# Kernel tuning notes

Hardware: AMD Instinct MI355X
Metric: run time of the kernel (lower is better)

Reference implementation:

```python
import jax, jax.numpy as jnp
import numpy as np

B, T, V, E = 1024, 100, 9173, 100
H1, H2 = 128, 512


def _gru(x, k, rk, b):
    # Keras GRU v2 (reset_after=True). x: [B,T,D], k: [D,3H], rk: [H,3H], b: [2,3H]
    bi, br = b[0], b[1]
    xs = jnp.swapaxes(jnp.einsum('btd,dh->bth', x, k) + bi, 0, 1)  # [T,B,3H]
    H = rk.shape[0]
    h0 = jnp.zeros((x.shape[0], H), x.dtype)

    def step(h, xt):
        inner = h @ rk + br
        xz, xr, xh = jnp.split(xt, 3, -1)
        rz, rr, rh = jnp.split(inner, 3, -1)
        z = jax.nn.sigmoid(xz + rz)
        r = jax.nn.sigmoid(xr + rr)
        hh = jnp.tanh(xh + r * rh)
        h = z * h + (1.0 - z) * hh
        return h, h

    _, ys = jax.lax.scan(step, h0, xs)
    return jnp.swapaxes(ys, 0, 1)  # [B,T,H]


def _lstm(x, k, rk, b, reverse=False):
    # Keras LSTM, gate order i,f,c,o. x: [B,T,D], k: [D,4H], rk: [H,4H], b: [4H]
    if reverse:
        x = x[:, ::-1]
    xs = jnp.swapaxes(jnp.einsum('btd,dh->bth', x, k) + b, 0, 1)  # [T,B,4H]
    H = rk.shape[0]
    Bb = x.shape[0]
    carry0 = (jnp.zeros((Bb, H), x.dtype), jnp.zeros((Bb, H), x.dtype))

    def step(carry, xt):
        h, c = carry
        g = xt + h @ rk
        i, f, cc, o = jnp.split(g, 4, -1)
        c = jax.nn.sigmoid(f) * c + jax.nn.sigmoid(i) * jnp.tanh(cc)
        h = jax.nn.sigmoid(o) * jnp.tanh(c)
        return (h, c), h

    _, ys = jax.lax.scan(step, carry0, xs)
    ys = jnp.swapaxes(ys, 0, 1)
    if reverse:
        ys = ys[:, ::-1]  # Bidirectional re-reverses backward outputs
    return ys


def setup_inputs() -> dict:
    key = jax.random.key(0)
    ks = jax.random.split(key, 32)
    s = 0.05
    p = {}
    p['text'] = jax.random.randint(ks[0], (B, T), 0, V)
    p['upvote'] = jax.random.normal(ks[1], (B, 1), jnp.float32)
    p['emb'] = s * jax.random.normal(ks[2], (V, E), jnp.float32)
    # forward GRU(128)
    p['gf_k'] = s * jax.random.normal(ks[3], (E, 3 * H1), jnp.float32)
    p['gf_rk'] = s * jax.random.normal(ks[4], (H1, 3 * H1), jnp.float32)
    p['gf_b'] = s * jax.random.normal(ks[5], (2, 3 * H1), jnp.float32)
    # backward LSTM(128)
    p['lb_k'] = s * jax.random.normal(ks[6], (E, 4 * H1), jnp.float32)
    p['lb_rk'] = s * jax.random.normal(ks[7], (H1, 4 * H1), jnp.float32)
    p['lb_b'] = s * jax.random.normal(ks[8], (4 * H1,), jnp.float32)
    # GRU(512) on concat(256)
    p['g2_k'] = s * jax.random.normal(ks[9], (2 * H1, 3 * H2), jnp.float32)
    p['g2_rk'] = s * jax.random.normal(ks[10], (H2, 3 * H2), jnp.float32)
    p['g2_b'] = s * jax.random.normal(ks[11], (2, 3 * H2), jnp.float32)
    # LSTM(512)
    p['l2_k'] = s * jax.random.normal(ks[12], (H2, 4 * H2), jnp.float32)
    p['l2_rk'] = s * jax.random.normal(ks[13], (H2, 4 * H2), jnp.float32)
    p['l2_b'] = s * jax.random.normal(ks[14], (4 * H2,), jnp.float32)
    # dense heads
    p['fc1_w'] = s * jax.random.normal(ks[15], (1, 512), jnp.float32)
    p['fc1_b'] = jnp.zeros((512,), jnp.float32)
    p['d1_w'] = s * jax.random.normal(ks[16], (1024, 64), jnp.float32)
    p['d1_b'] = jnp.zeros((64,), jnp.float32)
    p['d2_w'] = s * jax.random.normal(ks[17], (64, 512), jnp.float32)
    p['d2_b'] = jnp.zeros((512,), jnp.float32)
    p['d3_w'] = s * jax.random.normal(ks[18], (512, 128), jnp.float32)
    p['d3_b'] = jnp.zeros((128,), jnp.float32)
    p['rat_w'] = s * jax.random.normal(ks[19], (128, 5), jnp.float32)
    p['rat_b'] = jnp.zeros((5,), jnp.float32)
    p['rec_w'] = s * jax.random.normal(ks[20], (128, 1), jnp.float32)
    p['rec_b'] = jnp.zeros((1,), jnp.float32)
    return p


def reference(text, upvote, emb, gf_k, gf_rk, gf_b, lb_k, lb_rk, lb_b,
              g2_k, g2_rk, g2_b, l2_k, l2_rk, l2_b,
              fc1_w, fc1_b, d1_w, d1_b, d2_w, d2_b, d3_w, d3_b,
              rat_w, rat_b, rec_w, rec_b):
    x = emb[text]                                   # [B,T,E]
    fwd = _gru(x, gf_k, gf_rk, gf_b)                # [B,T,128]
    bwd = _lstm(x, lb_k, lb_rk, lb_b, reverse=True)  # [B,T,128]
    x1 = jnp.concatenate([fwd, bwd], -1)            # [B,T,256]
    x1 = _gru(x1, g2_k, g2_rk, g2_b)                # [B,T,512]
    x1 = _lstm(x1, l2_k, l2_rk, l2_b)               # [B,T,512]
    x1 = jnp.mean(x1, axis=1)                       # GlobalAveragePooling1D
    x2 = jax.nn.relu(upvote @ fc1_w + fc1_b)        # [B,512]
    h = jnp.concatenate([x1, x2], -1)               # [B,1024]
    h = jax.nn.relu(h @ d1_w + d1_b)
    h = jax.nn.relu(h @ d2_w + d2_b)
    h = jax.nn.relu(h @ d3_w + d3_b)
    rating = jax.nn.softmax(h @ rat_w + rat_b, axis=-1)
    recommend = jax.nn.sigmoid(h @ rec_w + rec_b)
    return rating, recommend
```

## Files before the change

kernel.cpp:

```cpp
#include <hip/hip_runtime.h>

typedef __attribute__((ext_vector_type(8))) short bf16x8;
typedef __attribute__((ext_vector_type(4))) float f32x4;

#define MFMA(a, b, c) __builtin_amdgcn_mfma_f32_16x16x32_bf16((a), (b), (c), 0, 0, 0)

__device__ inline short f2bf(float f) {
  unsigned u = __builtin_bit_cast(unsigned, f);
  u += 0x7fffu + ((u >> 16) & 1u);
  return (short)(u >> 16);
}
__device__ inline float bf2f(short s) {
  unsigned u = ((unsigned)(unsigned short)s) << 16;
  return __builtin_bit_cast(float, u);
}
__device__ inline float sigm(float x) { return 1.f / (1.f + expf(-x)); }

#define VM_DRAIN() asm volatile("s_waitcnt vmcnt(0)" ::: "memory")

__device__ __forceinline__ void sc_load16(const char* g0, const char* g1,
                                          const char* l0, const char* l1,
                                          bf16x8* rg, bf16x8* rl) {
  asm volatile(
      "global_load_dwordx4 %0, %16, off sc0 sc1\n\t"
      "global_load_dwordx4 %1, %16, off offset:1024 sc0 sc1\n\t"
      "global_load_dwordx4 %2, %16, off offset:2048 sc0 sc1\n\t"
      "global_load_dwordx4 %3, %16, off offset:3072 sc0 sc1\n\t"
      "global_load_dwordx4 %4, %17, off sc0 sc1\n\t"
      "global_load_dwordx4 %5, %17, off offset:1024 sc0 sc1\n\t"
      "global_load_dwordx4 %6, %17, off offset:2048 sc0 sc1\n\t"
      "global_load_dwordx4 %7, %17, off offset:3072 sc0 sc1\n\t"
      "global_load_dwordx4 %8, %18, off sc0 sc1\n\t"
      "global_load_dwordx4 %9, %18, off offset:1024 sc0 sc1\n\t"
      "global_load_dwordx4 %10, %18, off offset:2048 sc0 sc1\n\t"
      "global_load_dwordx4 %11, %18, off offset:3072 sc0 sc1\n\t"
      "global_load_dwordx4 %12, %19, off sc0 sc1\n\t"
      "global_load_dwordx4 %13, %19, off offset:1024 sc0 sc1\n\t"
      "global_load_dwordx4 %14, %19, off offset:2048 sc0 sc1\n\t"
      "global_load_dwordx4 %15, %19, off offset:3072 sc0 sc1\n\t"
      "s_waitcnt vmcnt(0)"
      : "=&v"(rg[0]), "=&v"(rg[1]), "=&v"(rg[2]), "=&v"(rg[3]),
        "=&v"(rg[4]), "=&v"(rg[5]), "=&v"(rg[6]), "=&v"(rg[7]),
        "=&v"(rl[0]), "=&v"(rl[1]), "=&v"(rl[2]), "=&v"(rl[3]),
        "=&v"(rl[4]), "=&v"(rl[5]), "=&v"(rl[6]), "=&v"(rl[7])
      : "v"(g0), "v"(g1), "v"(l0), "v"(l1)
      : "memory");
}

__device__ __forceinline__ void store_short_sys(short* p, short v) {
  int vi = (int)(unsigned short)v;
  asm volatile("global_store_short %0, %1, off sc0 sc1" :: "v"(p), "v"(vi) : "memory");
}

#define B_SZ 1024
#define T_SZ 100

#define O_GFK   0u
#define O_GFRK  (O_GFK  + 98304u)
#define O_LBK   (O_GFRK + 98304u)
#define O_LBRK  (O_LBK  + 131072u)
#define O_G2    (O_LBRK + 131072u)
#define O_L2    (O_G2   + 2359296u)
#define O_X     (O_L2   + 4194304u)
#define O_X1    (O_X    + 26214400u)
#define O_HG    (O_X1   + 52428800u)
#define O_HL    (O_HG   + 2097152u)
#define O_BAR   (O_HL   + 2097152u)
#define O_MS    (O_BAR  + 2097152u)
#define O_HGH   (O_MS   + 2097152u)
#define O_HLH   (O_HGH  + 105906176u)
#define WS_NEED (O_HLH + 105906176u)

__global__ void pack_b(const float* __restrict__ s1, int K1,
                       const float* __restrict__ s2, int K1p,
                       int Kp, int N, short* __restrict__ dst) {
  int i = blockIdx.x * 256 + threadIdx.x;
  int total = N * Kp;
  if (i >= total) return;
  int v = i & 7, c = (i >> 3) & 15, r = i >> 7;
  int kb8 = Kp >> 3;
  int kb = r % kb8, nt = r / kb8;
  int k = kb * 8 + v, col = nt * 16 + c;
  float val;
  if (k < K1p) val = (k < K1) ? s1[k * N + col] : 0.f;
  else         val = s2[(k - K1p) * N + col];
  dst[i] = f2bf(val);
}

__global__ void embed_k(const int* __restrict__ text, const float* __restrict__ emb,
                        short* __restrict__ x) {
  int i = blockIdx.x * 256 + threadIdx.x;
  if (i >= B_SZ * T_SZ * 128) return;
  int col = i & 127, bt = i >> 7;
  float v = 0.f;
  if (col < 100) v = emb[text[bt] * 100 + col];
  x[i] = f2bf(v);
}

__global__ __launch_bounds__(512) void layer1_k(
    const short* __restrict__ x, const short* __restrict__ gfk,
    const short* __restrict__ gfrk, const float* __restrict__ gfb,
    const short* __restrict__ lbk, const short* __restrict__ lbrk,
    const float* __restrict__ lbb, short* __restrict__ x1) {
  __shared__ __attribute__((aligned(16))) short rkl[65536];
  __shared__ __attribute__((aligned(16))) short xst[16 * 136];
  __shared__ __attribute__((aligned(16))) short hst[16 * 136];
  const int wgid = blockIdx.x;
  const bool gru = wgid < 64;
  const int b0 = (gru ? wgid : wgid - 64) * 16;
  const int tid = threadIdx.x, lane = tid & 63, w = tid >> 6;
  const int c = lane & 15, g = lane >> 4;
  const int NS = gru ? 3 : 4;

  for (int i = tid; i < 16 * 136; i += 512) hst[i] = 0;

  const bf16x8* kp = (const bf16x8*)(gru ? gfk : lbk);
  const bf16x8* rpg = (const bf16x8*)(gru ? gfrk : lbrk);
  {
    bf16x8* rl8 = (bf16x8*)rkl;
    int n8 = gru ? 6144 : 8192;
    for (int i = tid; i < n8; i += 512) rl8[i] = rpg[i];
  }
  const bf16x8* rp = (const bf16x8*)rkl;

  bf16x8 kf[4][4];
  #pragma unroll
  for (int s = 0; s < 4; ++s)
    if (s < NS)
      #pragma unroll
      for (int ks = 0; ks < 4; ++ks)
        kf[s][ks] = kp[((s * 8 + w) * 16 + 4 * ks + g) * 16 + c];

  const int col = w * 16 + c;
  float bz = 0, br_ = 0, bxh = 0, brh = 0, bi_ = 0, bf_ = 0, bc_ = 0, bo_ = 0;
  if (gru) {
    bz  = gfb[col]       + gfb[384 + col];
    br_ = gfb[128 + col] + gfb[512 + col];
    bxh = gfb[256 + col];
    brh = gfb[640 + col];
  } else {
    bi_ = lbb[col]; bf_ = lbb[128 + col]; bc_ = lbb[256 + col]; bo_ = lbb[384 + col];
  }

  float hreg[4] = {0.f, 0.f, 0.f, 0.f};
  float cst[4]  = {0.f, 0.f, 0.f, 0.f};

  for (int tt = 0; tt < T_SZ; ++tt) {
    const int t = gru ? tt : (T_SZ - 1 - tt);
    __syncthreads();
    if (tid < 256) {
      int row = tid >> 4, ch = tid & 15;
      *(bf16x8*)&xst[row * 136 + ch * 8] =
          *(const bf16x8*)&x[((b0 + row) * T_SZ + t) * 128 + ch * 8];
    }
    __syncthreads();

    f32x4 acc[4];
    #pragma unroll
    for (int s = 0; s < 4; ++s) acc[s] = (f32x4){0.f, 0.f, 0.f, 0.f};

    bf16x8 ax[4], ah[4];
    #pragma unroll
    for (int ks = 0; ks < 4; ++ks) {
      ax[ks] = *(const bf16x8*)&xst[c * 136 + ks * 32 + g * 8];
      ah[ks] = *(const bf16x8*)&hst[c * 136 + ks * 32 + g * 8];
    }
    #pragma unroll
    for (int s = 0; s < 4; ++s) {
      if (s < NS) {
        int dst = (gru && s == 2) ? 3 : s;
        #pragma unroll
        for (int ks = 0; ks < 4; ++ks) {
          acc[s] = MFMA(ax[ks], kf[s][ks], acc[s]);
          bf16x8 bh = rp[((s * 8 + w) * 16 + 4 * ks + g) * 16 + c];
          acc[dst] = MFMA(ah[ks], bh, acc[dst]);
        }
      }
    }
    __syncthreads();

    if (gru) {
      #pragma unroll
      for (int j = 0; j < 4; ++j) {
        float z  = sigm(acc[0][j] + bz);
        float r  = sigm(acc[1][j] + br_);
        float hh = tanhf(acc[2][j] + bxh + r * (acc[3][j] + brh));
        float hn = z * hreg[j] + (1.f - z) * hh;
        hreg[j] = hn;
        short hb = f2bf(hn);
        int row = 4 * g + j;
        hst[row * 136 + col] = hb;
        x1[((b0 + row) * T_SZ + t) * 256 + col] = hb;
      }
    } else {
      #pragma unroll
      for (int j = 0; j < 4; ++j) {
        float i_ = acc[0][j] + bi_;
        float f_ = acc[1][j] + bf_;
        float cc = acc[2][j] + bc_;
        float o_ = acc[3][j] + bo_;
        float cn = sigm(f_) * cst[j] + sigm(i_) * tanhf(cc);
        cst[j] = cn;
        float hn = sigm(o_) * tanhf(cn);
        short hb = f2bf(hn);
        int row = 4 * g + j;
        hst[row * 136 + col] = hb;
        x1[((b0 + row) * T_SZ + t) * 256 + 128 + col] = hb;
      }
    }
  }
}

__device__ __forceinline__ void gbar16(unsigned* bar, int grp, int gen) {
  VM_DRAIN();
  __syncthreads();
  if (threadIdx.x == 0) {
    unsigned want = (unsigned)(gen + 1);
    unsigned* cnt = bar + grp * 32;
    unsigned* rel = cnt + 16;
    unsigned o = __hip_atomic_fetch_add(cnt, 1u, __ATOMIC_RELAXED, __HIP_MEMORY_SCOPE_AGENT);
    if (o == want * 16u - 1u) {
      __hip_atomic_store(rel, want, __ATOMIC_RELAXED, __HIP_MEMORY_SCOPE_AGENT);
    } else {
      unsigned tries = 0;
      while (__hip_atomic_load(rel, __ATOMIC_RELAXED, __HIP_MEMORY_SCOPE_AGENT) < want) {
        __builtin_amdgcn_s_sleep(2);
        if (++tries > (1u << 22)) break;
      }
    }
  }
  __syncthreads();
}

__global__ __launch_bounds__(512, 2) void persist2_k(
    const short* __restrict__ x1, const short* __restrict__ G2p, const float* __restrict__ g2b,
    const short* __restrict__ L2p, const float* __restrict__ l2b,
    short* __restrict__ hg, short* __restrict__ hl,
    short* __restrict__ hgH, short* __restrict__ hlH,
    float* __restrict__ msum, unsigned* __restrict__ bar, int mode) {
  __shared__ __attribute__((aligned(16))) short Asm[65536];
  float* XA  = (float*)Asm;
  float* XB  = (float*)&Asm[32768];

  const int wgid = blockIdx.x;
  const int rowwg = wgid & 15, colwg = wgid >> 4;
  const int b0 = rowwg * 64;
  const int tid = threadIdx.x, w = tid >> 6, lane = tid & 63;
  const int c = lane & 15, g = lane >> 4;
  const int c7 = c & 7;
  const int ehc = lane & 31;
  const int er0 = w * 8 + (lane >> 5) * 4;
  const int hcg = colwg * 32 + ehc;

  const float bz  = g2b[hcg] + g2b[1536 + hcg];
  const float br_ = g2b[512 + hcg] + g2b[2048 + hcg];
  const float bxh = g2b[1024 + hcg];
  const float brh = g2b[2560 + hcg];
  const float bi_ = l2b[hcg], bf_ = l2b[512 + hcg];
  const float bc_ = l2b[1024 + hcg], bo_ = l2b[1536 + hcg];

  const bf16x8* Gv  = (const bf16x8*)G2p;
  const bf16x8* L2v = (const bf16x8*)L2p;
  const int gw = w >> 1, ghf = w & 1;
  const int gntg = gw * 32 + colwg * 2 + ghf;
  const int lgate = w & 3, lkh = w >> 2;

  float creg[4] = {0.f, 0.f, 0.f, 0.f};
  float mreg[4] = {0.f, 0.f, 0.f, 0.f};

  for (int k = 0; k <= 100; ++k) {
    const short* hg_rd = mode ? hgH + (size_t)k * 524288
                              : hg + (size_t)((k + 1) & 1) * 524288;
    const short* hl_rd = mode ? hlH + (size_t)(k >= 1 ? k - 1 : 0) * 524288
                              : hl + (size_t)(k & 1) * 524288;

    if (k < 100) {
      const bf16x8* x1v = (const bf16x8*)x1;
      #pragma unroll
      for (int it = 0; it < 4; ++it) {
        int idx = it * 512 + tid;
        int row = idx >> 5, cx = idx & 31;
        *(bf16x8*)&Asm[32768 + row * 256 + ((cx ^ (row & 7)) << 3)] =
            x1v[((size_t)(b0 + row) * T_SZ + k) * 32 + cx];
      }
    }

    bf16x8 rg[8], rl[8];
    {
      const char* bg = (const char*)hg_rd + (size_t)(b0 + w * 8) * 1024 + (size_t)lane * 16;
      const char* bl = (const char*)hl_rd + (size_t)(b0 + w * 8) * 1024 + (size_t)lane * 16;
      if (mode) {
        #pragma unroll
        for (int q = 0; q < 8; ++q) rg[q] = *(const bf16x8*)(bg + q * 1024);
        #pragma unroll
        for (int q = 0; q < 8; ++q) rl[q] = *(const bf16x8*)(bl + q * 1024);
      } else {
        sc_load16(bg, bg + 4096, bl, bl + 4096, rg, rl);
      }
    }
    #pragma unroll
    for (int q = 0; q < 8; ++q)
      *(bf16x8*)&Asm[(w * 8 + q) * 512 + ((lane ^ q) << 3)] = rg[q];
    __syncthreads();

    if (k < 100) {
      f32x4 acc[4], acch[4];
      if (w < 6) {
        #pragma unroll
        for (int m = 0; m < 4; ++m) {
          acc[m] = (f32x4){0.f, 0.f, 0.f, 0.f};
          acch[m] = (f32x4){0.f, 0.f, 0.f, 0.f};
        }
        #pragma unroll 6
        for (int ks = 0; ks < 24; ++ks) {
          bf16x8 b = Gv[((size_t)gntg * 96 + 4 * ks + g) * 16 + c];
          bf16x8 a[4];
          #pragma unroll
          for (int m = 0; m < 4; ++m) {
            int row = m * 16 + c;
            a[m] = (ks < 8)
                ? *(const bf16x8*)&Asm[32768 + row * 256 + (((ks * 4 + g) ^ c7) << 3)]
                : *(const bf16x8*)&Asm[row * 512 + ((((ks - 8) * 4 + g) ^ c7) << 3)];
          }
          if (w >= 4 && ks >= 8) {
            #pragma unroll
            for (int m = 0; m < 4; ++m) acch[m] = MFMA(a[m], b, acch[m]);
          } else {
            #pragma unroll
            for (int m = 0; m < 4; ++m) acc[m] = MFMA(a[m], b, acc[m]);
          }
        }
      }
      __syncthreads();

      if (w < 6) {
        #pragma unroll
        for (int m = 0; m < 4; ++m)
          #pragma unroll
          for (int j = 0; j < 4; ++j) {
            int row = m * 16 + 4 * g + j;
            if (gw < 2) XB[(gw * 64 + row) * 36 + ghf * 16 + c] = acc[m][j];
            else {
              XB[(128 + row) * 36 + ghf * 16 + c] = acc[m][j];
              XB[(192 + row) * 36 + ghf * 16 + c] = acch[m][j];
            }
          }
      }
      __syncthreads();

      short* hgw = mode ? hgH + (size_t)(k + 1) * 524288
                        : hg + (size_t)(k & 1) * 524288;
      #pragma unroll
      for (int j = 0; j < 4; ++j) {
        int r = er0 + j;
        int xi = r * 36 + ehc;
        float z  = sigm(XB[xi] + bz);
        float rr = sigm(XB[xi + 2304] + br_);
        float hh = tanhf(XB[xi + 4608] + bxh + rr * (XB[xi + 6912] + brh));
        float hold = bf2f(Asm[r * 512 + (((hcg >> 3) ^ (r & 7)) << 3) + (hcg & 7)]);
        float hn = z * hold + (1.f - z) * hh;
        store_short_sys(&hgw[(size_t)(b0 + r) * 512 + hcg], f2bf(hn));
      }
      __syncthreads();
    }

    if (k >= 1) {
      #pragma unroll
      for (int q = 0; q < 8; ++q)
        *(bf16x8*)&Asm[32768 + (w * 8 + q) * 512 + ((lane ^ q) << 3)] = rl[q];
      __syncthreads();

      f32x4 acc[4][2];
      #pragma unroll
      for (int m = 0; m < 4; ++m)
        #pragma unroll
        for (int n = 0; n < 2; ++n) acc[m][n] = (f32x4){0.f, 0.f, 0.f, 0.f};

      const int abase = lkh ? 32768 : 0;
      #pragma unroll
      for (int ks = 0; ks < 16; ++ks) {
        bf16x8 a[4];
        #pragma unroll
        for (int m = 0; m < 4; ++m) {
          int row = m * 16 + c;
          a[m] = *(const bf16x8*)&Asm[abase + row * 512 + (((ks * 4 + g) ^ c7) << 3)];
        }
        #pragma unroll
        for (int m = 0; m < 4; ++m)
          #pragma unroll
          for (int n = 0; n < 2; ++n) {
            bf16x8 b = L2v[((size_t)(lgate * 32 + colwg * 2 + n) * 128 +
                            4 * (lkh * 16 + ks) + g) * 16 + c];
            acc[m][n] = MFMA(a[m], b, acc[m][n]);
          }
      }
      __syncthreads();

      float* Xp = lkh ? XB : XA;
      #pragma unroll
      for (int m = 0; m < 4; ++m)
        #pragma unroll
        for (int n = 0; n < 2; ++n)
          #pragma unroll
          for (int j = 0; j < 4; ++j)
            Xp[(lgate * 64 + m * 16 + 4 * g + j) * 36 + n * 16 + c] = acc[m][n][j];
      __syncthreads();

      short* hlw = mode ? hlH + (size_t)k * 524288
                        : hl + (size_t)((k + 1) & 1) * 524288;
      #pragma unroll
      for (int j = 0; j < 4; ++j) {
        int r = er0 + j;
        int xi = r * 36 + ehc;
        float i_ = XA[xi]        + XB[xi]        + bi_;
        float f_ = XA[xi + 2304] + XB[xi + 2304] + bf_;
        float cc = XA[xi + 4608] + XB[xi + 4608] + bc_;
        float o_ = XA[xi + 6912] + XB[xi + 6912] + bo_;
        float cn = sigm(f_) * creg[j] + sigm(i_) * tanhf(cc);
        creg[j] = cn;
        float hn = sigm(o_) * tanhf(cn);
        mreg[j] += hn;
        store_short_sys(&hlw[(size_t)(b0 + r) * 512 + hcg], f2bf(hn));
      }
    }

    gbar16(bar, rowwg, k);
  }

  #pragma unroll
  for (int j = 0; j < 4; ++j)
    msum[(size_t)(b0 + er0 + j) * 512 + hcg] = mreg[j];
}

__global__ __launch_bounds__(256) void head_k(
    const float* __restrict__ msum, const float* __restrict__ upv,
    const float* __restrict__ fc1w, const float* __restrict__ fc1b,
    const float* __restrict__ d1w, const float* __restrict__ d1b,
    const float* __restrict__ d2w, const float* __restrict__ d2b,
    const float* __restrict__ d3w, const float* __restrict__ d3b,
    const float* __restrict__ rw, const float* __restrict__ rb,
    const float* __restrict__ cw, const float* __restrict__ cb,
    float* __restrict__ out) {
  __shared__ float h[1024], o1[64], o2[512], o3[128], lg[8];
  const int b = blockIdx.x, tid = threadIdx.x;
  const float u = upv[b];
  for (int i = tid; i < 512; i += 256) {
    h[i] = msum[b * 512 + i] * 0.01f;
    float v = u * fc1w[i] + fc1b[i];
    h[512 + i] = v > 0.f ? v : 0.f;
  }
  __syncthreads();
  if (tid < 64) {
    float a = d1b[tid];
    for (int i = 0; i < 1024; ++i) a += h[i] * d1w[i * 64 + tid];
    o1[tid] = a > 0.f ? a : 0.f;
  }
  __syncthreads();
  for (int j = tid; j < 512; j += 256) {
    float a = d2b[j];
    for (int i = 0; i < 64; ++i) a += o1[i] * d2w[i * 512 + j];
    o2[j] = a > 0.f ? a : 0.f;
  }
  __syncthreads();
  if (tid < 128) {
    float a = d3b[tid];
    for (int i = 0; i < 512; ++i) a += o2[i] * d3w[i * 128 + tid];
    o3[tid] = a > 0.f ? a : 0.f;
  }
  __syncthreads();
  if (tid < 5) {
    float a = rb[tid];
    for (int i = 0; i < 128; ++i) a += o3[i] * rw[i * 5 + tid];
    lg[tid] = a;
  }
  if (tid == 5) {
    float a = cb[0];
    for (int i = 0; i < 128; ++i) a += o3[i] * cw[i];
    out[5120 + b] = 1.f / (1.f + expf(-a));
  }
  __syncthreads();
  if (tid == 0) {
    float m = lg[0];
    for (int j = 1; j < 5; ++j) m = fmaxf(m, lg[j]);
    float e[5], s = 0.f;
    for (int j = 0; j < 5; ++j) { e[j] = expf(lg[j] - m); s += e[j]; }
    for (int j = 0; j < 5; ++j) out[b * 5 + j] = e[j] / s;
  }
}

extern "C" void kernel_launch(void* const* d_in, const int* in_sizes, int n_in,
                              void* d_out, int out_size, void* d_ws, size_t ws_size,
                              hipStream_t stream) {
  const int*   text  = (const int*)  d_in[0];
  const float* upv   = (const float*)d_in[1];
  const float* emb   = (const float*)d_in[2];
  const float* gf_k  = (const float*)d_in[3];
  const float* gf_rk = (const float*)d_in[4];
  const float* gf_b  = (const float*)d_in[5];
  const float* lb_k  = (const float*)d_in[6];
  const float* lb_rk = (const float*)d_in[7];
  const float* lb_b  = (const float*)d_in[8];
  const float* g2_k  = (const float*)d_in[9];
  const float* g2_rk = (const float*)d_in[10];
  const float* g2_b  = (const float*)d_in[11];
  const float* l2_k  = (const float*)d_in[12];
  const float* l2_rk = (const float*)d_in[13];
  const float* l2_b  = (const float*)d_in[14];
  const float* fc1_w = (const float*)d_in[15];
  const float* fc1_b = (const float*)d_in[16];
  const float* d1_w  = (const float*)d_in[17];
  const float* d1_b  = (const float*)d_in[18];
  const float* d2_w  = (const float*)d_in[19];
  const float* d2_b  = (const float*)d_in[20];
  const float* d3_w  = (const float*)d_in[21];
  const float* d3_b  = (const float*)d_in[22];
  const float* rat_w = (const float*)d_in[23];
  const float* rat_b = (const float*)d_in[24];
  const float* rec_w = (const float*)d_in[25];
  const float* rec_b = (const float*)d_in[26];

  char* ws = (char*)d_ws;
  short* gfkp  = (short*)(ws + O_GFK);
  short* gfrkp = (short*)(ws + O_GFRK);
  short* lbkp  = (short*)(ws + O_LBK);
  short* lbrkp = (short*)(ws + O_LBRK);
  short* G2p   = (short*)(ws + O_G2);
  short* L2p   = (short*)(ws + O_L2);
  short* xb    = (short*)(ws + O_X);
  short* x1    = (short*)(ws + O_X1);
  short* hg    = (short*)(ws + O_HG);
  short* hl    = (short*)(ws + O_HL);
  unsigned* bar = (unsigned*)(ws + O_BAR);
  float* msum  = (float*)(ws + O_MS);
  short* hgH   = (short*)(ws + O_HGH);
  short* hlH   = (short*)(ws + O_HLH);

  const int mode = (ws_size >= (size_t)WS_NEED) ? 1 : 0;

  pack_b<<<192, 256, 0, stream>>>(gf_k, 100, gf_k, 128, 128, 384, gfkp);
  pack_b<<<192, 256, 0, stream>>>(gf_rk, 128, gf_rk, 128, 128, 384, gfrkp);
  pack_b<<<256, 256, 0, stream>>>(lb_k, 100, lb_k, 128, 128, 512, lbkp);
  pack_b<<<256, 256, 0, stream>>>(lb_rk, 128, lb_rk, 128, 128, 512, lbrkp);
  pack_b<<<4608, 256, 0, stream>>>(g2_k, 256, g2_rk, 256, 768, 1536, G2p);
  pack_b<<<8192, 256, 0, stream>>>(l2_k, 512, l2_rk, 512, 1024, 2048, L2p);

  embed_k<<<51200, 256, 0, stream>>>(text, emb, xb);

  hipMemsetAsync(ws + O_BAR, 0, 4096u, stream);
  if (mode) {
    hipMemsetAsync(ws + O_HGH, 0, 1048576u, stream);
    hipMemsetAsync(ws + O_HLH, 0, 1048576u, stream);
  } else {
    hipMemsetAsync(ws + O_HG + 1048576u, 0, 1048576u, stream);
    hipMemsetAsync(ws + O_HL + 1048576u, 0, 1048576u, stream);
  }

  layer1_k<<<128, 512, 0, stream>>>(xb, gfkp, gfrkp, gf_b, lbkp, lbrkp, lb_b, x1);

  {
    const short* x1c = x1; const short* G2c = G2p; const short* L2c = L2p;
    int modec = mode;
    void* kargs[] = {(void*)&x1c, (void*)&G2c, (void*)&g2_b, (void*)&L2c, (void*)&l2_b,
                     (void*)&hg, (void*)&hl, (void*)&hgH, (void*)&hlH,
                     (void*)&msum, (void*)&bar, (void*)&modec};
    hipError_t e = hipLaunchCooperativeKernel((void*)persist2_k, dim3(256), dim3(512),
                                              kargs, 0, stream);
    if (e != hipSuccess) {
      (void)hipGetLastError();
      persist2_k<<<256, 512, 0, stream>>>(x1c, G2c, g2_b, L2c, l2_b, hg, hl, hgH, hlH,
                                          msum, bar, modec);
    }
  }

  head_k<<<1024, 256, 0, stream>>>(msum, upv, fc1_w, fc1_b, d1_w, d1_b, d2_w, d2_b,
                                   d3_w, d3_b, rat_w, rat_b, rec_w, rec_b,
                                   (float*)d_out);
}
```

Before: 2.989 ms.

## Merge GRU and LSTM recurrent phases into one stage with fewer barriers

Restructures the persistent layer-2 step so the GRU and LSTM recurrent matmuls run together after a single shared-memory staging of both hidden states. Work is redistributed across all 8 waves, and LSTM waves now do the full K reduction instead of splitting it in halves. The per-step x1 slice is read straight from global memory into the MFMA operands rather than staged through LDS. This cuts the number of __syncthreads per timestep and removes a partial-sum add, but the GRU work is now unevenly split across waves and the MFMA loops are no longer explicitly unrolled.

Measured after the change: 2.885 ms, median of 3. -3.5%, faster.

```diff
diff --git a/kernel.cpp b/kernel.cpp
--- a/kernel.cpp
+++ b/kernel.cpp
@@ -239,8 +239,8 @@
     short* __restrict__ hgH, short* __restrict__ hlH,
     float* __restrict__ msum, unsigned* __restrict__ bar, int mode) {
   __shared__ __attribute__((aligned(16))) short Asm[65536];
-  float* XA  = (float*)Asm;
-  float* XB  = (float*)&Asm[32768];
+  float* XFg = (float*)Asm;
+  float* XFl = ((float*)Asm) + 9216;
 
   const int wgid = blockIdx.x;
   const int rowwg = wgid & 15, colwg = wgid >> 4;
@@ -261,9 +261,16 @@
 
   const bf16x8* Gv  = (const bf16x8*)G2p;
   const bf16x8* L2v = (const bf16x8*)L2p;
-  const int gw = w >> 1, ghf = w & 1;
-  const int gntg = gw * 32 + colwg * 2 + ghf;
-  const int lgate = w & 3, lkh = w >> 2;
+  const bf16x8* x1v = (const bf16x8*)x1;
+
+  const int lgate = w >> 1, ln = w & 1;
+  const int lntg  = lgate * 32 + colwg * 2 + ln;
+  const int gslot = (w < 4) ? (w >> 1) : (2 + ((w >> 1) & 1));
+  const int gnt   = w & 1;
+  const int gbase = (gslot == 0) ? 0 : (gslot == 1) ? 32 : 64;
+  const int gntg  = gbase + colwg * 2 + gnt;
+  const int gks0  = (gslot == 3) ? 8 : 0;
+  const int gksN  = (gslot == 2) ? 8 : 24;
 
   float creg[4] = {0.f, 0.f, 0.f, 0.f};
   float mreg[4] = {0.f, 0.f, 0.f, 0.f};
@@ -274,17 +281,6 @@
     const short* hl_rd = mode ? hlH + (size_t)(k >= 1 ? k - 1 : 0) * 524288
                               : hl + (size_t)(k & 1) * 524288;
 
-    if (k < 100) {
-      const bf16x8* x1v = (const bf16x8*)x1;
-      #pragma unroll
-      for (int it = 0; it < 4; ++it) {
-        int idx = it * 512 + tid;
-        int row = idx >> 5, cx = idx & 31;
-        *(bf16x8*)&Asm[32768 + row * 256 + ((cx ^ (row & 7)) << 3)] =
-            x1v[((size_t)(b0 + row) * T_SZ + k) * 32 + cx];
-      }
-    }
-
     bf16x8 rg[8], rl[8];
     {
       const char* bg = (const char*)hg_rd + (size_t)(b0 + w * 8) * 1024 + (size_t)lane * 16;
@@ -301,121 +297,96 @@
     #pragma unroll
     for (int q = 0; q < 8; ++q)
       *(bf16x8*)&Asm[(w * 8 + q) * 512 + ((lane ^ q) << 3)] = rg[q];
+    #pragma unroll
+    for (int q = 0; q < 8; ++q)
+      *(bf16x8*)&Asm[32768 + (w * 8 + q) * 512 + ((lane ^ q) << 3)] = rl[q];
     __syncthreads();
 
+    f32x4 ga[4], la[4];
+    #pragma unroll
+    for (int m = 0; m < 4; ++m) {
+      ga[m] = (f32x4){0.f, 0.f, 0.f, 0.f};
+      la[m] = (f32x4){0.f, 0.f, 0.f, 0.f};
+    }
+
     if (k < 100) {
-      f32x4 acc[4], acch[4];
-      if (w < 6) {
+      for (int ks = gks0; ks < gksN; ++ks) {
+        bf16x8 b = Gv[((size_t)gntg * 96 + 4 * ks + g) * 16 + c];
         #pragma unroll
         for (int m = 0; m < 4; ++m) {
-          acc[m] = (f32x4){0.f, 0.f, 0.f, 0.f};
-          acch[m] = (f32x4){0.f, 0.f, 0.f, 0.f};
+          bf16x8 a;
+          if (ks < 8)
+            a = x1v[((size_t)(b0 + m * 16 + c) * T_SZ + k) * 32 + ks * 4 + g];
+          else
+            a = *(const bf16x8*)&Asm[(m * 16 + c) * 512 + ((((ks - 8) * 4 + g) ^ c7) << 3)];
+          ga[m] = MFMA(a, b, ga[m]);
         }
-        #pragma unroll 6
-        for (int ks = 0; ks < 24; ++ks) {
-          bf16x8 b = Gv[((size_t)gntg * 96 + 4 * ks + g) * 16 + c];
-          bf16x8 a[4];
-          #pragma unroll
-          for (int m = 0; m < 4; ++m) {
-            int row = m * 16 + c;
-            a[m] = (ks < 8)
-                ? *(const bf16x8*)&Asm[32768 + row * 256 + (((ks * 4 + g) ^ c7) << 3)]
-                : *(const bf16x8*)&Asm[row * 512 + ((((ks - 8) * 4 + g) ^ c7) << 3)];
-          }
-          if (w >= 4 && ks >= 8) {
-            #pragma unroll
-            for (int m = 0; m < 4; ++m) acch[m] = MFMA(a[m], b, acch[m]);
-          } else {
-            #pragma unroll
-            for (int m = 0; m < 4; ++m) acc[m] = MFMA(a[m], b, acc[m]);
-          }
+      }
+    }
+    if (k >= 1) {
+      for (int ks = 0; ks < 32; ++ks) {
+        bf16x8 b = L2v[((size_t)lntg * 128 + 4 * ks + g) * 16 + c];
+        #pragma unroll
+        for (int m = 0; m < 4; ++m) {
+          bf16x8 a = (ks < 16)
+              ? *(const bf16x8*)&Asm[(m * 16 + c) * 512 + (((ks * 4 + g) ^ c7) << 3)]
+              : *(const bf16x8*)&Asm[32768 + (m * 16 + c) * 512 + ((((ks - 16) * 4 + g) ^ c7) << 3)];
+          la[m] = MFMA(a, b, la[m]);
         }
       }
-      __syncthreads();
-
-      if (w < 6) {
-        #pragma unroll
-        for (int m = 0; m < 4; ++m)
-          #pragma unroll
-          for (int j = 0; j < 4; ++j) {
-            int row = m * 16 + 4 * g + j;
-            if (gw < 2) XB[(gw * 64 + row) * 36 + ghf * 16 + c] = acc[m][j];
-            else {
-              XB[(128 + row) * 36 + ghf * 16 + c] = acc[m][j];
-              XB[(192 + row) * 36 + ghf * 16 + c] = acch[m][j];
-            }
-          }
-      }
-      __syncthreads();
-
+    }
+
+    float hold[4];
+    if (k < 100) {
+      #pragma unroll
+      for (int j = 0; j < 4; ++j) {
+        int r = er0 + j;
+        hold[j] = bf2f(Asm[r * 512 + (((hcg >> 3) ^ (r & 7)) << 3) + (hcg & 7)]);
+      }
+    }
+    __syncthreads();
+
+    if (k < 100) {
+      #pragma unroll
+      for (int m = 0; m < 4; ++m)
+        #pragma unroll
+        for (int j = 0; j < 4; ++j)
+          XFg[(gslot * 64 + m * 16 + 4 * g + j) * 36 + gnt * 16 + c] = ga[m][j];
+    }
+    if (k >= 1) {
+      #pragma unroll
+      for (int m = 0; m < 4; ++m)
+        #pragma unroll
+        for (int j = 0; j < 4; ++j)
+          XFl[(lgate * 64 + m * 16 + 4 * g + j) * 36 + ln * 16 + c] = la[m][j];
+    }
+    __syncthreads();
+
+    if (k < 100) {
       short* hgw = mode ? hgH + (size_t)(k + 1) * 524288
                         : hg + (size_t)(k & 1) * 524288;
       #pragma unroll
       for (int j = 0; j < 4; ++j) {
         int r = er0 + j;
         int xi = r * 36 + ehc;
-        float z  = sigm(XB[xi] + bz);
-        float rr = sigm(XB[xi + 2304] + br_);
-        float hh = tanhf(XB[xi + 4608] + bxh + rr * (XB[xi + 6912] + brh));
-        float hold = bf2f(Asm[r * 512 + (((hcg >> 3) ^ (r & 7)) << 3) + (hcg & 7)]);
-        float hn = z * hold + (1.f - z) * hh;
+        float z  = sigm(XFg[xi] + bz);
+        float rr = sigm(XFg[2304 + xi] + br_);
+        float hh = tanhf(XFg[4608 + xi] + bxh + rr * (XFg[6912 + xi] + brh));
+        float hn = z * hold[j] + (1.f - z) * hh;
         store_short_sys(&hgw[(size_t)(b0 + r) * 512 + hcg], f2bf(hn));
       }
-      __syncthreads();
-    }
-
+    }
     if (k >= 1) {
-      #pragma unroll
-      for (int q = 0; q < 8; ++q)
-        *(bf16x8*)&Asm[32768 + (w * 8 + q) * 512 + ((lane ^ q) << 3)] = rl[q];
-      __syncthreads();
-
-      f32x4 acc[4][2];
-      #pragma unroll
-      for (int m = 0; m < 4; ++m)
-        #pragma unroll
-        for (int n = 0; n < 2; ++n) acc[m][n] = (f32x4){0.f, 0.f, 0.f, 0.f};
-
-      const int abase = lkh ? 32768 : 0;
-      #pragma unroll
-      for (int ks = 0; ks < 16; ++ks) {
-        bf16x8 a[4];
-        #pragma unroll
-        for (int m = 0; m < 4; ++m) {
-          int row = m * 16 + c;
-          a[m] = *(const bf16x8*)&Asm[abase + row * 512 + (((ks * 4 + g) ^ c7) << 3)];
-        }
-        #pragma unroll
-        for (int m = 0; m < 4; ++m)
-          #pragma unroll
-          for (int n = 0; n < 2; ++n) {
-            bf16x8 b = L2v[((size_t)(lgate * 32 + colwg * 2 + n) * 128 +
-                            4 * (lkh * 16 + ks) + g) * 16 + c];
-            acc[m][n] = MFMA(a[m], b, acc[m][n]);
-          }
-      }
-      __syncthreads();
-
-      float* Xp = lkh ? XB : XA;
-      #pragma unroll
-      for (int m = 0; m < 4; ++m)
-        #pragma unroll
-        for (int n = 0; n < 2; ++n)
-          #pragma unroll
-          for (int j = 0; j < 4; ++j)
-            Xp[(lgate * 64 + m * 16 + 4 * g + j) * 36 + n * 16 + c] = acc[m][n][j];
-      __syncthreads();
-
       short* hlw = mode ? hlH + (size_t)k * 524288
                         : hl + (size_t)((k + 1) & 1) * 524288;
       #pragma unroll
       for (int j = 0; j < 4; ++j) {
         int r = er0 + j;
         int xi = r * 36 + ehc;
-        float i_ = XA[xi]        + XB[xi]        + bi_;
-        float f_ = XA[xi + 2304] + XB[xi + 2304] + bf_;
-        float cc = XA[xi + 4608] + XB[xi + 4608] + bc_;
-        float o_ = XA[xi + 6912] + XB[xi + 6912] + bo_;
+        float i_ = XFl[xi]        + bi_;
+        float f_ = XFl[2304 + xi] + bf_;
+        float cc = XFl[4608 + xi] + bc_;
+        float o_ = XFl[6912 + xi] + bo_;
         float cn = sigm(f_) * creg[j] + sigm(i_) * tanhf(cc);
         creg[j] = cn;
         float hn = sigm(o_) * tanhf(cn);
```
